# Performance work log

Hardware: AMD Instinct MI355X
Metric: run time of the kernel (lower is better)

## Reference

```python
import jax, jax.numpy as jnp
import numpy as np

N_PATCHES = 14  # per side -> 196 patches

def patchify(images, n_patches):
    # images: [n, c, h, w]; returns [n, n_patches**2, c*ps*ps] with flatten order (c, ph, pw)
    n, c, h, w = images.shape
    ps = h // n_patches
    x = images.reshape(n, c, n_patches, ps, n_patches, ps)
    x = x.transpose(0, 2, 4, 1, 3, 5)  # [n, np_i, np_j, c, ps, ps]
    return x.reshape(n, n_patches * n_patches, c * ps * ps)

def setup_inputs() -> dict:
    key = jax.random.key(0)
    k1, k2, k3, k4 = jax.random.split(key, 4)
    B, C, H, Wd = 64, 3, 224, 224
    input_d = C * (H // N_PATCHES) * (Wd // N_PATCHES)  # 768
    hidden_d = 768
    images = jax.random.normal(k1, (B, C, H, Wd), dtype=jnp.float32)
    W = jax.random.normal(k2, (hidden_d, input_d), dtype=jnp.float32) * (1.0 / np.sqrt(input_d))
    b = jax.random.normal(k3, (hidden_d,), dtype=jnp.float32) * 0.01
    class_token = jax.random.uniform(k4, (1, hidden_d), dtype=jnp.float32)
    return {"images": images, "W": W, "b": b, "class_token": class_token}

def reference(images, W, b, class_token):
    patches = patchify(images, N_PATCHES)               # [B, 196, 768]
    tokens = jnp.einsum('bpd,hd->bph', patches, W) + b  # linear_mapper
    B = tokens.shape[0]
    cls = jnp.broadcast_to(class_token[None, :, :], (B, 1, class_token.shape[-1]))
    return jnp.concatenate([cls, tokens], axis=1)       # [B, 197, hidden_d]
```

## Files before the change

kernel.cpp:

```cpp
#include <hip/hip_runtime.h>
#include <cstdint>
#include <cstddef>

#define MTOT 12544
#define KTOT 768
#define NTOT 768

typedef float  f32x4  __attribute__((ext_vector_type(4)));
typedef __bf16 bf16x8 __attribute__((ext_vector_type(8)));

#define IMG_ELEMS (64*3*224*224)
#define W_ELEMS   (768*768)
#define A_BLOCKS  (IMG_ELEMS/8/256)
#define W_BLOCKS  (W_ELEMS/8/256)
#define CLS_BLOCKS 48

__global__ __launch_bounds__(256) void prep_kernel(
    const float* __restrict__ images, const float* __restrict__ Wm,
    const float* __restrict__ cls, float* __restrict__ out,
    __bf16* __restrict__ imgb, __bf16* __restrict__ Wb) {
  const int bid = blockIdx.x, tid = threadIdx.x;
  if (bid < A_BLOCKS) {
    const size_t q = (size_t)bid * 256 + tid;
    const float4 v0 = *(const float4*)(images + q * 8);
    const float4 v1 = *(const float4*)(images + q * 8 + 4);
    bf16x8 o;
    o[0]=(__bf16)v0.x; o[1]=(__bf16)v0.y; o[2]=(__bf16)v0.z; o[3]=(__bf16)v0.w;
    o[4]=(__bf16)v1.x; o[5]=(__bf16)v1.y; o[6]=(__bf16)v1.z; o[7]=(__bf16)v1.w;
    *(bf16x8*)(imgb + q * 8) = o;
  } else if (bid < A_BLOCKS + W_BLOCKS) {
    const size_t q = (size_t)(bid - A_BLOCKS) * 256 + tid;
    const float4 v0 = *(const float4*)(Wm + q * 8);
    const float4 v1 = *(const float4*)(Wm + q * 8 + 4);
    bf16x8 o;
    o[0]=(__bf16)v0.x; o[1]=(__bf16)v0.y; o[2]=(__bf16)v0.z; o[3]=(__bf16)v0.w;
    o[4]=(__bf16)v1.x; o[5]=(__bf16)v1.y; o[6]=(__bf16)v1.z; o[7]=(__bf16)v1.w;
    *(bf16x8*)(Wb + q * 8) = o;
  } else {
    const int t  = (bid - A_BLOCKS - W_BLOCKS) * 256 + tid;
    const int bb = t / 192;
    const int r  = t - bb * 192;
    *(float4*)(out + (size_t)bb * 197 * 768 + r * 4) = *(const float4*)(cls + r * 4);
  }
}

#define BM 64
#define BN 128
#define BK 64
#define NBLK_N 6

__device__ __forceinline__ void gload_lds16(const void* g, void* l) {
  __builtin_amdgcn_global_load_lds((__attribute__((address_space(1))) void*)(g),
                                   (__attribute__((address_space(3))) void*)(l),
                                   16, 0, 0);
}

__global__ __launch_bounds__(256) void gemm_kernel(
    const __bf16* __restrict__ imgb, const __bf16* __restrict__ Wb,
    const float* __restrict__ bias, float* __restrict__ out) {
  __shared__ __bf16 As[2 * 64 * 32];
  __shared__ __bf16 Bs[2 * 128 * 32];

  const int tid  = threadIdx.x;
  const int bx   = blockIdx.x;
  const int mblk = bx / NBLK_N;
  const int nblk = bx - mblk * NBLK_N;
  const int m0 = mblk * BM;
  const int n0 = nblk * BN;
  const int wave = tid >> 6, lane = tid & 63;
  const int wm = (wave & 1) * 32;
  const int wn = (wave >> 1) * 64;
  const int lrow = lane & 15, lq = lane >> 4;

  f32x4 acc[2][4] = {};

  const __bf16* pA[2];
#pragma unroll
  for (int s = 0; s < 2; ++s) {
    const int c = wave * 128 + s * 64 + lane;
    const int kstep = c >> 8, rem = c & 255;
    const int row = rem >> 2, jc = rem & 3;
    const int m = m0 + row;
    const int bb = m / 196, p = m - bb * 196;
    const int pi = p / 14, pj = p - pi * 14;
    const int ph_off = kstep * 2 + (jc >> 1);
    const int pw_off = (jc & 1) * 8;
    const size_t e = ((size_t)(bb * 3 * 224 + pi * 16 + ph_off)) * 224 + pj * 16 + pw_off;
    pA[s] = imgb + e;
  }
  const __bf16* pB[4];
#pragma unroll
  for (int s = 0; s < 4; ++s) {
    const int c = wave * 256 + s * 64 + lane;
    const int kstep = c >> 9, rem = c & 511;
    const int h = rem >> 2, jc = rem & 3;
    pB[s] = Wb + (size_t)(n0 + h) * 768 + kstep * 32 + jc * 8;
  }
  __bf16* lA[2];
  __bf16* lB[4];
#pragma unroll
  for (int s = 0; s < 2; ++s) lA[s] = As + (wave * 128 + s * 64) * 8;
#pragma unroll
  for (int s = 0; s < 4; ++s) lB[s] = Bs + (wave * 256 + s * 64) * 8;

  for (int kt = 0; kt < KTOT / BK; ++kt) {
#pragma unroll
    for (int s = 0; s < 2; ++s) gload_lds16(pA[s], lA[s]);
#pragma unroll
    for (int s = 0; s < 4; ++s) gload_lds16(pB[s], lB[s]);
    const int dA = ((kt & 3) == 3) ? 47488 : 896;
    pA[0] += dA; pA[1] += dA;
    pB[0] += BK; pB[1] += BK; pB[2] += BK; pB[3] += BK;
    __syncthreads();

#pragma unroll
    for (int ks = 0; ks < 2; ++ks) {
      bf16x8 af[2], bf[4];
#pragma unroll
      for (int i = 0; i < 2; ++i)
        af[i] = *(const bf16x8*)&As[ks * 2048 + (wm + i * 16 + lrow) * 32 + lq * 8];
#pragma unroll
      for (int j = 0; j < 4; ++j)
        bf[j] = *(const bf16x8*)&Bs[ks * 4096 + (wn + j * 16 + lrow) * 32 + lq * 8];
#pragma unroll
      for (int i = 0; i < 2; ++i)
#pragma unroll
        for (int j = 0; j < 4; ++j)
          acc[i][j] = __builtin_amdgcn_mfma_f32_16x16x32_bf16(af[i], bf[j], acc[i][j], 0, 0, 0);
    }
    __syncthreads();
  }

#pragma unroll
  for (int j = 0; j < 4; ++j) {
    const int h  = n0 + wn + j * 16 + lrow;
    const float bv = bias[h];
#pragma unroll
    for (int i = 0; i < 2; ++i) {
      const int mb = m0 + wm + i * 16 + lq * 4;
#pragma unroll
      for (int r = 0; r < 4; ++r) {
        const int m  = mb + r;
        const int bb = m / 196, p = m - bb * 196;
        out[(size_t)(bb * 197 + 1 + p) * 768 + h] = acc[i][j][r] + bv;
      }
    }
  }
}

extern "C" void kernel_launch(void* const* d_in, const int* in_sizes, int n_in,
                              void* d_out, int out_size, void* d_ws, size_t ws_size,
                              hipStream_t stream) {
  const float* images = (const float*)d_in[0];
  const float* Wm     = (const float*)d_in[1];
  const float* b      = (const float*)d_in[2];
  const float* cls    = (const float*)d_in[3];
  float* out = (float*)d_out;

  __bf16* imgb = (__bf16*)d_ws;
  __bf16* Wb   = imgb + (size_t)IMG_ELEMS;
  (void)in_sizes; (void)n_in; (void)out_size; (void)ws_size;

  prep_kernel<<<A_BLOCKS + W_BLOCKS + CLS_BLOCKS, 256, 0, stream>>>(
      images, Wm, cls, out, imgb, Wb);
  gemm_kernel<<<(MTOT / BM) * NBLK_N, 256, 0, stream>>>(imgb, Wb, b, out);
}
```

Before: 118.3 us.

## Fuse image fp32-to-bf16 conversion into GEMM A-tile loads

The separate pass that converts the whole image tensor to bf16 in workspace is removed. The GEMM now reads fp32 image rows directly, converts them in registers and writes padded LDS rows, which avoids a full write and re-read of the bf16 image copy. Block indices are also remapped so that neighbouring blocks spread across XCDs, and the A LDS rows are padded to reduce bank conflicts. In exchange the A loads are synchronous register loads rather than async global-to-LDS copies, and each N-block re-reads fp32 images, doubling the A read volume per block.

New measurement: 124.8 us. +5.5%, slower.

```diff
diff --git a/kernel.cpp b/kernel.cpp
--- a/kernel.cpp
+++ b/kernel.cpp
@@ -4,32 +4,19 @@
 
 #define MTOT 12544
 #define KTOT 768
-#define NTOT 768
 
 typedef float  f32x4  __attribute__((ext_vector_type(4)));
 typedef __bf16 bf16x8 __attribute__((ext_vector_type(8)));
 
-#define IMG_ELEMS (64*3*224*224)
-#define W_ELEMS   (768*768)
-#define A_BLOCKS  (IMG_ELEMS/8/256)
-#define W_BLOCKS  (W_ELEMS/8/256)
+#define W_BLOCKS   288
 #define CLS_BLOCKS 48
 
 __global__ __launch_bounds__(256) void prep_kernel(
-    const float* __restrict__ images, const float* __restrict__ Wm,
-    const float* __restrict__ cls, float* __restrict__ out,
-    __bf16* __restrict__ imgb, __bf16* __restrict__ Wb) {
+    const float* __restrict__ Wm, const float* __restrict__ cls,
+    float* __restrict__ out, __bf16* __restrict__ Wb) {
   const int bid = blockIdx.x, tid = threadIdx.x;
-  if (bid < A_BLOCKS) {
+  if (bid < W_BLOCKS) {
     const size_t q = (size_t)bid * 256 + tid;
-    const float4 v0 = *(const float4*)(images + q * 8);
-    const float4 v1 = *(const float4*)(images + q * 8 + 4);
-    bf16x8 o;
-    o[0]=(__bf16)v0.x; o[1]=(__bf16)v0.y; o[2]=(__bf16)v0.z; o[3]=(__bf16)v0.w;
-    o[4]=(__bf16)v1.x; o[5]=(__bf16)v1.y; o[6]=(__bf16)v1.z; o[7]=(__bf16)v1.w;
-    *(bf16x8*)(imgb + q * 8) = o;
-  } else if (bid < A_BLOCKS + W_BLOCKS) {
-    const size_t q = (size_t)(bid - A_BLOCKS) * 256 + tid;
     const float4 v0 = *(const float4*)(Wm + q * 8);
     const float4 v1 = *(const float4*)(Wm + q * 8 + 4);
     bf16x8 o;
@@ -37,7 +24,7 @@
     o[4]=(__bf16)v1.x; o[5]=(__bf16)v1.y; o[6]=(__bf16)v1.z; o[7]=(__bf16)v1.w;
     *(bf16x8*)(Wb + q * 8) = o;
   } else {
-    const int t  = (bid - A_BLOCKS - W_BLOCKS) * 256 + tid;
+    const int t  = (bid - W_BLOCKS) * 256 + tid;
     const int bb = t / 192;
     const int r  = t - bb * 192;
     *(float4*)(out + (size_t)bb * 197 * 768 + r * 4) = *(const float4*)(cls + r * 4);
@@ -46,7 +33,7 @@
 
 #define BM 64
 #define BN 128
-#define BK 64
+#define APAD 40
 #define NBLK_N 6
 
 __device__ __forceinline__ void gload_lds16(const void* g, void* l) {
@@ -56,61 +43,56 @@
 }
 
 __global__ __launch_bounds__(256) void gemm_kernel(
-    const __bf16* __restrict__ imgb, const __bf16* __restrict__ Wb,
+    const float* __restrict__ images, const __bf16* __restrict__ Wb,
     const float* __restrict__ bias, float* __restrict__ out) {
-  __shared__ __bf16 As[2 * 64 * 32];
-  __shared__ __bf16 Bs[2 * 128 * 32];
+  __shared__ __bf16 As[2 * BM * APAD];
+  __shared__ __bf16 Bs[2 * BN * 32];
 
-  const int tid  = threadIdx.x;
-  const int bx   = blockIdx.x;
-  const int mblk = bx / NBLK_N;
-  const int nblk = bx - mblk * NBLK_N;
-  const int m0 = mblk * BM;
-  const int n0 = nblk * BN;
+  const int tid = threadIdx.x;
+  const int g    = (blockIdx.x & 7) * 147 + (blockIdx.x >> 3);
+  const int mblk = g / NBLK_N, nblk = g - mblk * NBLK_N;
+  const int m0 = mblk * BM, n0 = nblk * BN;
   const int wave = tid >> 6, lane = tid & 63;
-  const int wm = (wave & 1) * 32;
-  const int wn = (wave >> 1) * 64;
+  const int wm = (wave & 1) * 32, wn = (wave >> 1) * 64;
   const int lrow = lane & 15, lq = lane >> 4;
+
+  const int row = lane;
+  const int m  = m0 + row;
+  const int bb = m / 196, p = m - bb * 196;
+  const int pi = p / 14,  pj = p - pi * 14;
+  const float* gA = images +
+      ((size_t)(bb * 3) * 224 + (size_t)(pi * 16 + wave)) * 224 + pj * 16;
+  const int aks = wave >> 1, akoff = (wave & 1) * 16;
+  __bf16* wA = &As[(aks * BM + row) * APAD + akoff];
+
+  const __bf16* pB[4];
+  __bf16* lB[4];
+#pragma unroll
+  for (int s = 0; s < 4; ++s) {
+    const int c  = wave * 256 + s * 64 + lane;
+    const int ks = c >> 9, rem = c & 511, h = rem >> 2, jc = rem & 3;
+    pB[s] = Wb + (size_t)(n0 + h) * 768 + ks * 32 + jc * 8;
+    lB[s] = Bs + (size_t)(wave * 256 + s * 64) * 8;
+  }
 
   f32x4 acc[2][4] = {};
 
-  const __bf16* pA[2];
-#pragma unroll
-  for (int s = 0; s < 2; ++s) {
-    const int c = wave * 128 + s * 64 + lane;
-    const int kstep = c >> 8, rem = c & 255;
-    const int row = rem >> 2, jc = rem & 3;
-    const int m = m0 + row;
-    const int bb = m / 196, p = m - bb * 196;
-    const int pi = p / 14, pj = p - pi * 14;
-    const int ph_off = kstep * 2 + (jc >> 1);
-    const int pw_off = (jc & 1) * 8;
-    const size_t e = ((size_t)(bb * 3 * 224 + pi * 16 + ph_off)) * 224 + pj * 16 + pw_off;
-    pA[s] = imgb + e;
-  }
-  const __bf16* pB[4];
-#pragma unroll
-  for (int s = 0; s < 4; ++s) {
-    const int c = wave * 256 + s * 64 + lane;
-    const int kstep = c >> 9, rem = c & 511;
-    const int h = rem >> 2, jc = rem & 3;
-    pB[s] = Wb + (size_t)(n0 + h) * 768 + kstep * 32 + jc * 8;
-  }
-  __bf16* lA[2];
-  __bf16* lB[4];
-#pragma unroll
-  for (int s = 0; s < 2; ++s) lA[s] = As + (wave * 128 + s * 64) * 8;
-#pragma unroll
-  for (int s = 0; s < 4; ++s) lB[s] = Bs + (wave * 256 + s * 64) * 8;
-
-  for (int kt = 0; kt < KTOT / BK; ++kt) {
-#pragma unroll
-    for (int s = 0; s < 2; ++s) gload_lds16(pA[s], lA[s]);
+  for (int kt = 0; kt < 12; ++kt) {
 #pragma unroll
     for (int s = 0; s < 4; ++s) gload_lds16(pB[s], lB[s]);
-    const int dA = ((kt & 3) == 3) ? 47488 : 896;
-    pA[0] += dA; pA[1] += dA;
-    pB[0] += BK; pB[1] += BK; pB[2] += BK; pB[3] += BK;
+    const float4 v0 = *(const float4*)(gA);
+    const float4 v1 = *(const float4*)(gA + 4);
+    const float4 v2 = *(const float4*)(gA + 8);
+    const float4 v3 = *(const float4*)(gA + 12);
+    bf16x8 o0, o1;
+    o0[0]=(__bf16)v0.x; o0[1]=(__bf16)v0.y; o0[2]=(__bf16)v0.z; o0[3]=(__bf16)v0.w;
+    o0[4]=(__bf16)v1.x; o0[5]=(__bf16)v1.y; o0[6]=(__bf16)v1.z; o0[7]=(__bf16)v1.w;
+    o1[0]=(__bf16)v2.x; o1[1]=(__bf16)v2.y; o1[2]=(__bf16)v2.z; o1[3]=(__bf16)v2.w;
+    o1[4]=(__bf16)v3.x; o1[5]=(__bf16)v3.y; o1[6]=(__bf16)v3.z; o1[7]=(__bf16)v3.w;
+    *(bf16x8*)(wA)     = o0;
+    *(bf16x8*)(wA + 8) = o1;
+    gA += ((kt & 3) == 3) ? 47488 : 896;
+    pB[0] += 64; pB[1] += 64; pB[2] += 64; pB[3] += 64;
     __syncthreads();
 
 #pragma unroll
@@ -118,10 +100,10 @@
       bf16x8 af[2], bf[4];
 #pragma unroll
       for (int i = 0; i < 2; ++i)
-        af[i] = *(const bf16x8*)&As[ks * 2048 + (wm + i * 16 + lrow) * 32 + lq * 8];
+        af[i] = *(const bf16x8*)&As[(ks * BM + wm + i * 16 + lrow) * APAD + lq * 8];
 #pragma unroll
       for (int j = 0; j < 4; ++j)
-        bf[j] = *(const bf16x8*)&Bs[ks * 4096 + (wn + j * 16 + lrow) * 32 + lq * 8];
+        bf[j] = *(const bf16x8*)&Bs[(ks * BN + wn + j * 16 + lrow) * 32 + lq * 8];
 #pragma unroll
       for (int i = 0; i < 2; ++i)
 #pragma unroll
@@ -140,9 +122,9 @@
       const int mb = m0 + wm + i * 16 + lq * 4;
 #pragma unroll
       for (int r = 0; r < 4; ++r) {
-        const int m  = mb + r;
-        const int bb = m / 196, p = m - bb * 196;
-        out[(size_t)(bb * 197 + 1 + p) * 768 + h] = acc[i][j][r] + bv;
+        const int mm  = mb + r;
+        const int bb2 = mm / 196, p2 = mm - bb2 * 196;
+        out[(size_t)(bb2 * 197 + 1 + p2) * 768 + h] = acc[i][j][r] + bv;
       }
     }
   }
@@ -156,12 +138,9 @@
   const float* b      = (const float*)d_in[2];
   const float* cls    = (const float*)d_in[3];
   float* out = (float*)d_out;
-
-  __bf16* imgb = (__bf16*)d_ws;
-  __bf16* Wb   = imgb + (size_t)IMG_ELEMS;
+  __bf16* Wb = (__bf16*)d_ws;
   (void)in_sizes; (void)n_in; (void)out_size; (void)ws_size;
 
-  prep_kernel<<<A_BLOCKS + W_BLOCKS + CLS_BLOCKS, 256, 0, stream>>>(
-      images, Wm, cls, out, imgb, Wb);
-  gemm_kernel<<<(MTOT / BM) * NBLK_N, 256, 0, stream>>>(imgb, Wb, b, out);
+  prep_kernel<<<W_BLOCKS + CLS_BLOCKS, 256, 0, stream>>>(Wm, cls, out, Wb);
+  gemm_kernel<<<(MTOT / BM) * NBLK_N, 256, 0, stream>>>(images, Wb, b, out);
 }
```
